# Optimization experiments

Hardware: AMD Instinct MI355X
Metric: run time of the kernel (lower is better)

Reference implementation:

```python
import jax, jax.numpy as jnp
import numpy as np
import math

KEY_SIZE = 64

def setup_inputs() -> dict:
    key = jax.random.key(0)
    kq, kk, kv, km = jax.random.split(key, 4)
    B, H, S, Dk, Dv = 4, 12, 2048, 64, 64
    Q = jax.random.normal(kq, (B, H, S, Dk), dtype=jnp.float32)
    K = jax.random.normal(kk, (B, H, S, Dk), dtype=jnp.float32)
    V = jax.random.normal(kv, (B, H, S, Dv), dtype=jnp.float32)
    mask_out = (jax.random.uniform(km, (B, H, 1, S)) < 0.9).astype(jnp.float32)
    return {"Q": Q, "K": K, "V": V, "mask_out": mask_out}

def reference(Q, K, V, mask_out):
    scale = math.sqrt(KEY_SIZE)
    # [B,H,Sq,Sk] scores
    scores = jnp.einsum('bhqd,bhkd->bhqk', Q, K) / scale
    attn = jax.nn.softmax(scores, axis=-1)
    attn = mask_out * attn  # post-softmax multiplicative mask (dropout=0)
    return jnp.einsum('bhqk,bhkv->bhqv', attn, V)
```

## Files before the change

kernel.cpp:

```cpp
#include <hip/hip_runtime.h>


typedef _Float16 f16x8 __attribute__((ext_vector_type(8)));
typedef _Float16 f16x4 __attribute__((ext_vector_type(4)));
typedef _Float16 f16x2 __attribute__((ext_vector_type(2)));
typedef float    f32x4 __attribute__((ext_vector_type(4)));

#define SEQ  2048
#define DIM  64
#define KT   64
#define LDSP 72
#define NIT  (SEQ / KT)

__device__ inline f16x8 cvt8(float4 a, float4 b) {
    return (f16x8){(_Float16)a.x,(_Float16)a.y,(_Float16)a.z,(_Float16)a.w,
                   (_Float16)b.x,(_Float16)b.y,(_Float16)b.z,(_Float16)b.w};
}
__device__ inline f16x8 cvt8s(float4 a, float4 b, float s) {
    return (f16x8){(_Float16)(a.x*s),(_Float16)(a.y*s),(_Float16)(a.z*s),(_Float16)(a.w*s),
                   (_Float16)(b.x*s),(_Float16)(b.y*s),(_Float16)(b.z*s),(_Float16)(b.w*s)};
}

__global__ __launch_bounds__(256, 3)
void fa_kernel(const float* __restrict__ Q, const float* __restrict__ K,
               const float* __restrict__ V, const float* __restrict__ Mask,
               float* __restrict__ Out)
{
    __shared__ _Float16 Kld[KT][LDSP];
    __shared__ _Float16 Vt[DIM][LDSP];

    const int bx    = blockIdx.x;
    const int head  = bx % 48;
    const int qtile = bx / 48;
    const int tid   = threadIdx.x;
    const int wave  = tid >> 6;
    const int lane  = tid & 63;
    const int quad  = lane >> 4;
    const int r     = lane & 15;

    const size_t hoff = (size_t)head * SEQ * DIM;
    const float* Qh = Q + hoff;
    const float* Kh = K + hoff;
    const float* Vh = V + hoff;
    const float* Mh = Mask + (size_t)head * SEQ;
    float* Oh = Out + hoff;

    const int qbase = qtile * 128 + wave * 32;
    const float c = 0.18033688011112042f;

    f16x8 qf[2][2];
    #pragma unroll
    for (int t = 0; t < 2; ++t) {
        const float* qrow = Qh + (size_t)(qbase + t * 16 + r) * DIM;
        #pragma unroll
        for (int kb = 0; kb < 2; ++kb) {
            const float4* p4 = (const float4*)(qrow + kb * 32 + quad * 8);
            qf[t][kb] = cvt8s(p4[0], p4[1], c);
        }
    }

    f32x4 o[4][2], ol[2];
    #pragma unroll
    for (int d = 0; d < 4; ++d)
        #pragma unroll
        for (int t = 0; t < 2; ++t) o[d][t] = (f32x4){0.f, 0.f, 0.f, 0.f};
    ol[0] = (f32x4){0.f, 0.f, 0.f, 0.f};
    ol[1] = (f32x4){0.f, 0.f, 0.f, 0.f};

    const f16x8 ones8 = {(_Float16)1.f,(_Float16)1.f,(_Float16)1.f,(_Float16)1.f,
                         (_Float16)1.f,(_Float16)1.f,(_Float16)1.f,(_Float16)1.f};

    const int skey = tid >> 2;
    const int sdb  = (tid & 3) * 16;
    const int srow = ((skey >> 5) << 5) + (((skey & 7) < 4) ? 0 : 16)
                   + (((skey & 31) >> 3) << 2) + (skey & 3);
    const int vk0  = (tid & 31) * 2;
    const int vdb  = (tid >> 5) * 8;

    float4 kr0, kr1, kr2, kr3, va0, va1, vb0, vb1;
    float mk0, mk1;
    auto load_tile = [&](int kbase) {
        const float4* kg = (const float4*)(Kh + (size_t)(kbase + skey) * DIM + sdb);
        kr0 = kg[0]; kr1 = kg[1]; kr2 = kg[2]; kr3 = kg[3];
        const float4* vg0 = (const float4*)(Vh + (size_t)(kbase + vk0) * DIM + vdb);
        const float4* vg1 = (const float4*)(Vh + (size_t)(kbase + vk0 + 1) * DIM + vdb);
        va0 = vg0[0]; va1 = vg0[1];
        vb0 = vg1[0]; vb1 = vg1[1];
        mk0 = Mh[kbase + vk0]; mk1 = Mh[kbase + vk0 + 1];
    };
    load_tile(0);

    for (int kbi = 0; kbi < NIT; ++kbi) {
        __syncthreads();
        *(f16x8*)&Kld[srow][sdb]     = cvt8(kr0, kr1);
        *(f16x8*)&Kld[srow][sdb + 8] = cvt8(kr2, kr3);
        {
            float va[8] = {va0.x, va0.y, va0.z, va0.w, va1.x, va1.y, va1.z, va1.w};
            float vb[8] = {vb0.x, vb0.y, vb0.z, vb0.w, vb1.x, vb1.y, vb1.z, vb1.w};
            #pragma unroll
            for (int j = 0; j < 8; ++j) {
                f16x2 w = {(_Float16)(va[j] * mk0), (_Float16)(vb[j] * mk1)};
                *(f16x2*)&Vt[vdb + j][vk0] = w;
            }
        }
        __syncthreads();

        if (kbi + 1 < NIT) load_tile((kbi + 1) * KT);

        f16x8 bfrag[2][2];
        #pragma unroll
        for (int g = 0; g < 2; ++g) {
            #pragma unroll
            for (int u = 0; u < 2; ++u) {
                const int ti = g * 2 + u;
                f16x8 kf0 = *(const f16x8*)&Kld[ti * 16 + r][quad * 8];
                f16x8 kf1 = *(const f16x8*)&Kld[ti * 16 + r][32 + quad * 8];
                #pragma unroll
                for (int t = 0; t < 2; ++t) {
                    f32x4 acc = (f32x4){-8.f, -8.f, -8.f, -8.f};
                    acc = __builtin_amdgcn_mfma_f32_16x16x32_f16(kf0, qf[t][0], acc, 0, 0, 0);
                    acc = __builtin_amdgcn_mfma_f32_16x16x32_f16(kf1, qf[t][1], acc, 0, 0, 0);
                    #pragma unroll
                    for (int i = 0; i < 4; ++i)
                        bfrag[g][t][u * 4 + i] =
                            (_Float16)__builtin_amdgcn_exp2f(acc[i]);
                }
            }
        }

        #pragma unroll
        for (int g = 0; g < 2; ++g) {
            ol[0] = __builtin_amdgcn_mfma_f32_16x16x32_f16(ones8, bfrag[g][0], ol[0], 0, 0, 0);
            ol[1] = __builtin_amdgcn_mfma_f32_16x16x32_f16(ones8, bfrag[g][1], ol[1], 0, 0, 0);
        }

        #pragma unroll
        for (int d = 0; d < 4; ++d) {
            #pragma unroll
            for (int g = 0; g < 2; ++g) {
                f16x8 vfrag = *(const f16x8*)&Vt[d * 16 + r][g * 32 + quad * 8];
                o[d][0] = __builtin_amdgcn_mfma_f32_16x16x32_f16(vfrag, bfrag[g][0], o[d][0], 0, 0, 0);
                o[d][1] = __builtin_amdgcn_mfma_f32_16x16x32_f16(vfrag, bfrag[g][1], o[d][1], 0, 0, 0);
            }
        }
    }

    #pragma unroll
    for (int t = 0; t < 2; ++t) {
        float inv = 1.0f / ol[t][0];
        const size_t rowoff = (size_t)(qbase + t * 16 + r) * DIM;
        #pragma unroll
        for (int d = 0; d < 4; ++d) {
            float4 v = {o[d][t][0] * inv, o[d][t][1] * inv,
                        o[d][t][2] * inv, o[d][t][3] * inv};
            *(float4*)&Oh[rowoff + d * 16 + quad * 4] = v;
        }
    }
}

extern "C" void kernel_launch(void* const* d_in, const int* in_sizes, int n_in,
                              void* d_out, int out_size, void* d_ws, size_t ws_size,
                              hipStream_t stream) {
    const float* Q = (const float*)d_in[0];
    const float* K = (const float*)d_in[1];
    const float* V = (const float*)d_in[2];
    const float* M = (const float*)d_in[3];
    float* O = (float*)d_out;
    dim3 grid(768), block(256);
    hipLaunchKernelGGL(fa_kernel, grid, block, 0, stream, Q, K, V, M, O);
}
```

Baseline: 184.4 us.

## Double-buffer K/V shared memory tiles to overlap staging with MFMA compute

Splits the K and transposed-V shared-memory tiles into two buffers and restructures the loop so the next tile is staged into the alternate buffer while the current tile is being computed. This cuts the two barriers per iteration to one. The prefetch distance grows to two tiles ahead. The cost is double LDS usage (about 18KB per block), which may limit occupancy at the requested 3 blocks per CU, and more live registers while staging happens mid-body.

```diff
diff --git a/kernel.cpp b/kernel.cpp
--- a/kernel.cpp
+++ b/kernel.cpp
@@ -2,7 +2,6 @@
 
 
 typedef _Float16 f16x8 __attribute__((ext_vector_type(8)));
-typedef _Float16 f16x4 __attribute__((ext_vector_type(4)));
 typedef _Float16 f16x2 __attribute__((ext_vector_type(2)));
 typedef float    f32x4 __attribute__((ext_vector_type(4)));
 
@@ -26,8 +25,8 @@
                const float* __restrict__ V, const float* __restrict__ Mask,
                float* __restrict__ Out)
 {
-    __shared__ _Float16 Kld[KT][LDSP];
-    __shared__ _Float16 Vt[DIM][LDSP];
+    __shared__ _Float16 Kld[2][KT][LDSP];
+    __shared__ _Float16 Vt[2][DIM][LDSP];
 
     const int bx    = blockIdx.x;
     const int head  = bx % 48;
@@ -88,33 +87,27 @@
         vb0 = vg1[0]; vb1 = vg1[1];
         mk0 = Mh[kbase + vk0]; mk1 = Mh[kbase + vk0 + 1];
     };
-    load_tile(0);
+    auto stage = [&](int p) {
+        *(f16x8*)&Kld[p][srow][sdb]     = cvt8(kr0, kr1);
+        *(f16x8*)&Kld[p][srow][sdb + 8] = cvt8(kr2, kr3);
+        float va[8] = {va0.x, va0.y, va0.z, va0.w, va1.x, va1.y, va1.z, va1.w};
+        float vb[8] = {vb0.x, vb0.y, vb0.z, vb0.w, vb1.x, vb1.y, vb1.z, vb1.w};
+        #pragma unroll
+        for (int j = 0; j < 8; ++j) {
+            f16x2 w = {(_Float16)(va[j] * mk0), (_Float16)(vb[j] * mk1)};
+            *(f16x2*)&Vt[p][vdb + j][vk0] = w;
+        }
+    };
 
-    for (int kbi = 0; kbi < NIT; ++kbi) {
-        __syncthreads();
-        *(f16x8*)&Kld[srow][sdb]     = cvt8(kr0, kr1);
-        *(f16x8*)&Kld[srow][sdb + 8] = cvt8(kr2, kr3);
-        {
-            float va[8] = {va0.x, va0.y, va0.z, va0.w, va1.x, va1.y, va1.z, va1.w};
-            float vb[8] = {vb0.x, vb0.y, vb0.z, vb0.w, vb1.x, vb1.y, vb1.z, vb1.w};
-            #pragma unroll
-            for (int j = 0; j < 8; ++j) {
-                f16x2 w = {(_Float16)(va[j] * mk0), (_Float16)(vb[j] * mk1)};
-                *(f16x2*)&Vt[vdb + j][vk0] = w;
-            }
-        }
-        __syncthreads();
-
-        if (kbi + 1 < NIT) load_tile((kbi + 1) * KT);
-
+    auto body = [&](int p, int kbi) {
         f16x8 bfrag[2][2];
         #pragma unroll
         for (int g = 0; g < 2; ++g) {
             #pragma unroll
             for (int u = 0; u < 2; ++u) {
                 const int ti = g * 2 + u;
-                f16x8 kf0 = *(const f16x8*)&Kld[ti * 16 + r][quad * 8];
-                f16x8 kf1 = *(const f16x8*)&Kld[ti * 16 + r][32 + quad * 8];
+                f16x8 kf0 = *(const f16x8*)&Kld[p][ti * 16 + r][quad * 8];
+                f16x8 kf1 = *(const f16x8*)&Kld[p][ti * 16 + r][32 + quad * 8];
                 #pragma unroll
                 for (int t = 0; t < 2; ++t) {
                     f32x4 acc = (f32x4){-8.f, -8.f, -8.f, -8.f};
@@ -128,21 +121,34 @@
             }
         }
 
+        if (kbi + 1 < NIT) stage(p ^ 1);
+        if (kbi + 2 < NIT) load_tile((kbi + 2) * KT);
+
         #pragma unroll
         for (int g = 0; g < 2; ++g) {
             ol[0] = __builtin_amdgcn_mfma_f32_16x16x32_f16(ones8, bfrag[g][0], ol[0], 0, 0, 0);
             ol[1] = __builtin_amdgcn_mfma_f32_16x16x32_f16(ones8, bfrag[g][1], ol[1], 0, 0, 0);
         }
-
         #pragma unroll
         for (int d = 0; d < 4; ++d) {
             #pragma unroll
             for (int g = 0; g < 2; ++g) {
-                f16x8 vfrag = *(const f16x8*)&Vt[d * 16 + r][g * 32 + quad * 8];
+                f16x8 vfrag = *(const f16x8*)&Vt[p][d * 16 + r][g * 32 + quad * 8];
                 o[d][0] = __builtin_amdgcn_mfma_f32_16x16x32_f16(vfrag, bfrag[g][0], o[d][0], 0, 0, 0);
                 o[d][1] = __builtin_amdgcn_mfma_f32_16x16x32_f16(vfrag, bfrag[g][1], o[d][1], 0, 0, 0);
             }
         }
+        __syncthreads();
+    };
+
+    load_tile(0);
+    stage(0);
+    load_tile(KT);
+    __syncthreads();
+
+    for (int kbi = 0; kbi < NIT; kbi += 2) {
+        body(0, kbi);
+        body(1, kbi + 1);
     }
 
     #pragma unroll
```

New measurement: 192.3 us. 1.04x slower.

## Split key tiles across wave pairs and reduce partial outputs through LDS

Applied to the files above, without the earlier changes.

Each block now covers 64 queries instead of 128, and the grid doubles. The four waves form two query halves times two key halves, and each wave processes half of every key tile. Partial numerators and denominators from the second key-half waves are combined through shared memory at the end. The goal is more blocks and parallelism (1536 blocks, up to 4 per CU) and lower per-wave register pressure, at the cost of loading K/V tiles twice as often per query and adding an epilogue reduction.

```diff
diff --git a/kernel.cpp b/kernel.cpp
--- a/kernel.cpp
+++ b/kernel.cpp
@@ -2,7 +2,6 @@
 
 
 typedef _Float16 f16x8 __attribute__((ext_vector_type(8)));
-typedef _Float16 f16x4 __attribute__((ext_vector_type(4)));
 typedef _Float16 f16x2 __attribute__((ext_vector_type(2)));
 typedef float    f32x4 __attribute__((ext_vector_type(4)));
 
@@ -21,13 +20,15 @@
                    (_Float16)(b.x*s),(_Float16)(b.y*s),(_Float16)(b.z*s),(_Float16)(b.w*s)};
 }
 
-__global__ __launch_bounds__(256, 3)
+__global__ __launch_bounds__(256, 4)
 void fa_kernel(const float* __restrict__ Q, const float* __restrict__ K,
                const float* __restrict__ V, const float* __restrict__ Mask,
                float* __restrict__ Out)
 {
     __shared__ _Float16 Kld[KT][LDSP];
     __shared__ _Float16 Vt[DIM][LDSP];
+    __shared__ float Ored[2][DIM][33];
+    __shared__ float Lred[2][2][16];
 
     const int bx    = blockIdx.x;
     const int head  = bx % 48;
@@ -37,6 +38,8 @@
     const int lane  = tid & 63;
     const int quad  = lane >> 4;
     const int r     = lane & 15;
+    const int kh    = wave >> 1;
+    const int qh    = wave & 1;
 
     const size_t hoff = (size_t)head * SEQ * DIM;
     const float* Qh = Q + hoff;
@@ -45,7 +48,7 @@
     const float* Mh = Mask + (size_t)head * SEQ;
     float* Oh = Out + hoff;
 
-    const int qbase = qtile * 128 + wave * 32;
+    const int qbase = qtile * 64 + qh * 32;
     const float c = 0.18033688011112042f;
 
     f16x8 qf[2][2];
@@ -107,53 +110,65 @@
 
         if (kbi + 1 < NIT) load_tile((kbi + 1) * KT);
 
-        f16x8 bfrag[2][2];
+        f16x8 bfrag[2];
         #pragma unroll
-        for (int g = 0; g < 2; ++g) {
+        for (int u = 0; u < 2; ++u) {
+            const int ti = kh * 2 + u;
+            f16x8 kf0 = *(const f16x8*)&Kld[ti * 16 + r][quad * 8];
+            f16x8 kf1 = *(const f16x8*)&Kld[ti * 16 + r][32 + quad * 8];
             #pragma unroll
-            for (int u = 0; u < 2; ++u) {
-                const int ti = g * 2 + u;
-                f16x8 kf0 = *(const f16x8*)&Kld[ti * 16 + r][quad * 8];
-                f16x8 kf1 = *(const f16x8*)&Kld[ti * 16 + r][32 + quad * 8];
+            for (int t = 0; t < 2; ++t) {
+                f32x4 acc = (f32x4){-8.f, -8.f, -8.f, -8.f};
+                acc = __builtin_amdgcn_mfma_f32_16x16x32_f16(kf0, qf[t][0], acc, 0, 0, 0);
+                acc = __builtin_amdgcn_mfma_f32_16x16x32_f16(kf1, qf[t][1], acc, 0, 0, 0);
                 #pragma unroll
-                for (int t = 0; t < 2; ++t) {
-                    f32x4 acc = (f32x4){-8.f, -8.f, -8.f, -8.f};
-                    acc = __builtin_amdgcn_mfma_f32_16x16x32_f16(kf0, qf[t][0], acc, 0, 0, 0);
-                    acc = __builtin_amdgcn_mfma_f32_16x16x32_f16(kf1, qf[t][1], acc, 0, 0, 0);
-                    #pragma unroll
-                    for (int i = 0; i < 4; ++i)
-                        bfrag[g][t][u * 4 + i] =
-                            (_Float16)__builtin_amdgcn_exp2f(acc[i]);
-                }
+                for (int i = 0; i < 4; ++i)
+                    bfrag[t][u * 4 + i] =
+                        (_Float16)__builtin_amdgcn_exp2f(acc[i]);
             }
         }
 
-        #pragma unroll
-        for (int g = 0; g < 2; ++g) {
-            ol[0] = __builtin_amdgcn_mfma_f32_16x16x32_f16(ones8, bfrag[g][0], ol[0], 0, 0, 0);
-            ol[1] = __builtin_amdgcn_mfma_f32_16x16x32_f16(ones8, bfrag[g][1], ol[1], 0, 0, 0);
-        }
+        ol[0] = __builtin_amdgcn_mfma_f32_16x16x32_f16(ones8, bfrag[0], ol[0], 0, 0, 0);
+        ol[1] = __builtin_amdgcn_mfma_f32_16x16x32_f16(ones8, bfrag[1], ol[1], 0, 0, 0);
 
         #pragma unroll
         for (int d = 0; d < 4; ++d) {
-            #pragma unroll
-            for (int g = 0; g < 2; ++g) {
-                f16x8 vfrag = *(const f16x8*)&Vt[d * 16 + r][g * 32 + quad * 8];
-                o[d][0] = __builtin_amdgcn_mfma_f32_16x16x32_f16(vfrag, bfrag[g][0], o[d][0], 0, 0, 0);
-                o[d][1] = __builtin_amdgcn_mfma_f32_16x16x32_f16(vfrag, bfrag[g][1], o[d][1], 0, 0, 0);
-            }
+            f16x8 vfrag = *(const f16x8*)&Vt[d * 16 + r][kh * 32 + quad * 8];
+            o[d][0] = __builtin_amdgcn_mfma_f32_16x16x32_f16(vfrag, bfrag[0], o[d][0], 0, 0, 0);
+            o[d][1] = __builtin_amdgcn_mfma_f32_16x16x32_f16(vfrag, bfrag[1], o[d][1], 0, 0, 0);
         }
     }
 
-    #pragma unroll
-    for (int t = 0; t < 2; ++t) {
-        float inv = 1.0f / ol[t][0];
-        const size_t rowoff = (size_t)(qbase + t * 16 + r) * DIM;
+    __syncthreads();
+    if (kh == 1) {
+        if (quad == 0) {
+            Lred[qh][0][r] = ol[0][0];
+            Lred[qh][1][r] = ol[1][0];
+        }
         #pragma unroll
-        for (int d = 0; d < 4; ++d) {
-            float4 v = {o[d][t][0] * inv, o[d][t][1] * inv,
-                        o[d][t][2] * inv, o[d][t][3] * inv};
-            *(float4*)&Oh[rowoff + d * 16 + quad * 4] = v;
+        for (int d = 0; d < 4; ++d)
+            #pragma unroll
+            for (int t = 0; t < 2; ++t)
+                #pragma unroll
+                for (int i = 0; i < 4; ++i)
+                    Ored[qh][d * 16 + quad * 4 + i][t * 16 + r] = o[d][t][i];
+    }
+    __syncthreads();
+    if (kh == 0) {
+        #pragma unroll
+        for (int t = 0; t < 2; ++t) {
+            float l = ol[t][0] + Lred[qh][t][r];
+            float inv = 1.0f / l;
+            const size_t rowoff = (size_t)(qbase + t * 16 + r) * DIM;
+            #pragma unroll
+            for (int d = 0; d < 4; ++d) {
+                float4 v;
+                v.x = (o[d][t][0] + Ored[qh][d * 16 + quad * 4 + 0][t * 16 + r]) * inv;
+                v.y = (o[d][t][1] + Ored[qh][d * 16 + quad * 4 + 1][t * 16 + r]) * inv;
+                v.z = (o[d][t][2] + Ored[qh][d * 16 + quad * 4 + 2][t * 16 + r]) * inv;
+                v.w = (o[d][t][3] + Ored[qh][d * 16 + quad * 4 + 3][t * 16 + r]) * inv;
+                *(float4*)&Oh[rowoff + d * 16 + quad * 4] = v;
+            }
         }
     }
 }
@@ -166,6 +181,6 @@
     const float* V = (const float*)d_in[2];
     const float* M = (const float*)d_in[3];
     float* O = (float*)d_out;
-    dim3 grid(768), block(256);
+    dim3 grid(1536), block(256);
     hipLaunchKernelGGL(fa_kernel, grid, block, 0, stream, Q, K, V, M, O);
 }
```

Result: slower. 246.0 us (+33.4%).
